# Performance work log

Hardware: AMD Instinct MI355X
Metric: run time of the kernel (lower is better)

Reference implementation:

```python
import jax, jax.numpy as jnp
import numpy as np

NX, NA, T = 128, 64, 1024
MU = 1.0          # self.mu at entry to backward_pass
EPS = 1e-8        # singular-value clamp (self.eps)


def setup_inputs() -> dict:
    key = jax.random.key(0)
    ks = jax.random.split(key, 7)
    sx = 0.3 / np.sqrt(NX)  # keep dynamics spectral norm < 1 so recursion is stable
    fx = jax.random.normal(ks[0], (T, NX, NX), dtype=jnp.float32) * sx
    fa = jax.random.normal(ks[1], (T, NX, NA), dtype=jnp.float32) * sx
    lx = jax.random.normal(ks[2], (T, NX), dtype=jnp.float32)
    la = jax.random.normal(ks[3], (T, NA), dtype=jnp.float32)
    A = jax.random.normal(ks[4], (T, NX, NX), dtype=jnp.float32) * 0.1
    lxx = 0.5 * (A + A.transpose(0, 2, 1)) + jnp.eye(NX, dtype=jnp.float32)
    B = jax.random.normal(ks[5], (T, NA, NA), dtype=jnp.float32) * 0.1
    laa = 0.5 * (B + B.transpose(0, 2, 1)) + jnp.eye(NA, dtype=jnp.float32)
    lax = jax.random.normal(ks[6], (T, NA, NX), dtype=jnp.float32) * 0.1
    return dict(fx=fx, fa=fa, lx=lx, la=la, lxx=lxx, laa=laa, lax=lax)


def reference(fx, fa, lx, la, lxx, laa, lax):
    """iLQR backward Riccati recursion (ILQR.backward_pass + ILQR.q).
    Returns gains [T, na, 1+nx]: column 0 is k (feedforward), columns 1: are K
    (feedback), ordered by ascending time t=0..T-1."""
    I = jnp.eye(NX, dtype=fx.dtype)

    def step(carry, inp):
        Vx, Vxx = carry
        fx_t, fa_t, lx_t, la_t, lxx_t, laa_t, lax_t = inp
        # Q-function expansion (ILQR.q)
        Qx = lx_t + fx_t.T @ Vx
        Qa = la_t + fa_t.T @ Vx
        Qxx = lxx_t + fx_t.T @ Vxx @ fx_t
        Vreg = Vxx + MU * I
        Qax = lax_t + fa_t.T @ Vreg @ fx_t
        Qaa = laa_t + fa_t.T @ Vreg @ fa_t
        # SVD-based regularized inverse (S[S<eps] = eps)
        U, S, Vh = jnp.linalg.svd(Qaa)
        S = jnp.maximum(S, EPS)
        Vm = Vh.T
        Qaa_inv = (Vm * (1.0 / S)) @ U.T   # V diag(1/S) U^T
        Qaa_r = (U * S) @ Vm.T             # U diag(S) V^T (reconstructed Qaa)
        k = -Qaa_inv @ Qa
        K = -Qaa_inv @ Qax
        # value-function recursion
        Vx_n = Qx + K.T @ (Qaa_r @ k) + K.T @ Qa + Qax.T @ k
        Vxx_n = Qxx + K.T @ Qaa_r @ K + K.T @ Qax + Qax.T @ K
        Vxx_n = 0.5 * (Vxx_n + Vxx_n.T)
        return (Vx_n, Vxx_n), jnp.concatenate([k[:, None], K], axis=1)

    init = (lx[-1], lxx[-1])  # terminal Vx, Vxx
    (_, _), gains = jax.lax.scan(step, init, (fx, fa, lx, la, lxx, laa, lax), reverse=True)
    return gains
```

## Files before the change

### kernel.cpp

```cpp
#include <hip/hip_runtime.h>
#include <math.h>

#define TSTEPS 1024
#define NXD 128
#define NAD 64
#define NBLK 64
#define LSTR 67
#define GAINW 129

__device__ __forceinline__ float rdl(float v, int l) {
  return __int_as_float(__builtin_amdgcn_readlane(__float_as_int(v), l));
}
__device__ __forceinline__ double rdl(double v, int l) {
  unsigned long long b = (unsigned long long)__double_as_longlong(v);
  int lo = __builtin_amdgcn_readlane((int)(b & 0xffffffffULL), l);
  int hi = __builtin_amdgcn_readlane((int)(b >> 32), l);
  unsigned long long r = (((unsigned long long)(unsigned)hi) << 32) | (unsigned)lo;
  return __longlong_as_double((long long)r);
}

__device__ __forceinline__ void gbar(unsigned* arrive, unsigned* epoch, unsigned e) {
  __syncthreads();
  if (threadIdx.x == 0) {
    unsigned prev = __hip_atomic_fetch_add(arrive, 1u, __ATOMIC_ACQ_REL, __HIP_MEMORY_SCOPE_AGENT);
    if (prev == e * NBLK - 1u) {
      __hip_atomic_store(epoch, e, __ATOMIC_RELEASE, __HIP_MEMORY_SCOPE_AGENT);
    } else {
      while (__hip_atomic_load(epoch, __ATOMIC_ACQUIRE, __HIP_MEMORY_SCOPE_AGENT) < e) {
        __builtin_amdgcn_s_sleep(1);
      }
    }
  }
  __syncthreads();
}

__device__ __forceinline__ float factor32(const float* __restrict__ QaaC, int lane,
                                          float* __restrict__ Lsh) {
  float a[64];
#pragma unroll
  for (int k = 0; k < 64; ++k) a[k] = QaaC[lane * NAD + k];
  float mmax = 0.f;
#pragma unroll
  for (int j = 0; j < 63; ++j) {
    float d = rdl(a[j], j);
    d = (d == 0.f) ? 1e-30f : d;
    float rdv = 1.0f / d;
    float m = a[j] * rdv;
    m = (lane > j) ? m : 0.f;
    mmax = fmaxf(mmax, fabsf(m));
#pragma unroll
    for (int k = j + 1; k < 64; ++k) {
      float u = rdl(a[j], k);
      a[k] = fmaf(-m, u, a[k]);
    }
    if (lane > j) a[j] = m;
  }
#pragma unroll
  for (int k = 0; k < 64; ++k) Lsh[lane * LSTR + k] = a[k];
#pragma unroll
  for (int s = 1; s < 64; s <<= 1) mmax = fmaxf(mmax, __shfl_xor(mmax, s));
  return mmax;
}

__device__ __forceinline__ void factor64(const float* __restrict__ QaaC, int lane,
                                         double* __restrict__ Lsh) {
  double a[64];
#pragma unroll
  for (int k = 0; k < 64; ++k) a[k] = (double)QaaC[lane * NAD + k];
#pragma unroll
  for (int j = 0; j < 63; ++j) {
    double d = rdl(a[j], j);
    d = (d == 0.0) ? 1e-300 : d;
    double rdv = 1.0 / d;
    double m = a[j] * rdv;
    m = (lane > j) ? m : 0.0;
#pragma unroll
    for (int k = j + 1; k < 64; ++k) {
      double u = rdl(a[j], k);
      a[k] = fma(-m, u, a[k]);
    }
    if (lane > j) a[j] = m;
  }
#pragma unroll
  for (int k = 0; k < 64; ++k) Lsh[lane * LSTR + k] = a[k];
}

template <typename T>
__device__ __forceinline__ void trisolve(const T* __restrict__ Lsh, int lane, float bval,
                                         float* __restrict__ gout, float* __restrict__ kout) {
  T x = (T)bval;
  for (int j = 0; j < 63; ++j) {
    T xj = rdl(x, j);
    T lij = Lsh[lane * LSTR + j];
    if (lane > j) x = x - lij * xj;
  }
  T d = Lsh[lane * LSTR + lane];
  if (d == (T)0) d = (T)1e-30;
  x = x / d;
  for (int j = 63; j > 0; --j) {
    T xj = rdl(x, j);
    T lji = Lsh[j * LSTR + lane];
    if (lane < j) x = x - lji * xj;
  }
  float g = -(float)x;
  *gout = g;
  *kout = g;
}

__device__ __forceinline__ void matvec128(const float* __restrict__ Vxx, float fcl, float fch,
                                          int lane, float& w0, float& w1) {
  w0 = 0.f; w1 = 0.f;
  const float* vrow = Vxx + 2 * lane;
#pragma unroll 8
  for (int c = 0; c < 64; ++c) {
    float s = rdl(fcl, c);
    float2 v = *(const float2*)(vrow + (size_t)c * NXD);
    w0 = fmaf(v.x, s, w0); w1 = fmaf(v.y, s, w1);
  }
#pragma unroll 8
  for (int c = 0; c < 64; ++c) {
    float s = rdl(fch, c);
    float2 v = *(const float2*)(vrow + (size_t)(64 + c) * NXD);
    w0 = fmaf(v.x, s, w0); w1 = fmaf(v.y, s, w1);
  }
}

__global__ void init_bar_kernel(unsigned* bar) {
  bar[threadIdx.x] = 0u;
}

__global__ __launch_bounds__(256, 1) void ilqr_main(
    const float* __restrict__ fx, const float* __restrict__ fa,
    const float* __restrict__ lx, const float* __restrict__ la,
    const float* __restrict__ lxx, const float* __restrict__ laa,
    const float* __restrict__ lax, float* __restrict__ out,
    float* __restrict__ wsf, unsigned* __restrict__ bar) {

  __shared__ float  LfS[64 * LSTR];
  __shared__ double LdS[64 * LSTR];
  __shared__ int flag64;

  const int b = blockIdx.x;
  const int tid = threadIdx.x;
  const int wave = tid >> 6;
  const int lane = tid & 63;

  float* Vxx  = wsf;
  float* Vx   = Vxx + 16384;
  float* QxxC = Vx + 128;
  float* QaxT = QxxC + 16384;
  float* QaaC = QaxT + 8192;
  float* Qx   = QaaC + 4096;
  float* Qa   = Qx + 128;
  float* KT   = Qa + 64;

  unsigned* arrive = bar;
  unsigned* epoch  = bar + 32;
  unsigned ep = 0;

  {
    const float* src = lxx + (size_t)(TSTEPS - 1) * NXD * NXD;
    int idx = b * 256 + tid;
    if (idx < NXD * NXD) Vxx[idx] = src[idx];
    if (b == 0 && tid < NXD) Vx[tid] = lx[(size_t)(TSTEPS - 1) * NXD + tid];
  }
  ++ep; gbar(arrive, epoch, ep);

  for (int t = TSTEPS - 1; t >= 0; --t) {
    const float* fxt  = fx  + (size_t)t * NXD * NXD;
    const float* fat  = fa  + (size_t)t * NXD * NAD;
    const float* lxt  = lx  + (size_t)t * NXD;
    const float* lat  = la  + (size_t)t * NAD;
    const float* lxxt = lxx + (size_t)t * NXD * NXD;
    const float* laat = laa + (size_t)t * NAD * NAD;
    const float* laxt = lax + (size_t)t * NAD * NXD;

    if (wave <= 1) {
      const int j = 2 * b + wave;
      float fcl = fxt[lane * NXD + j];
      float fch = fxt[(64 + lane) * NXD + j];
      float w0, w1;
      matvec128(Vxx, fcl, fch, lane, w0, w1);

      float q0 = lxxt[(size_t)(2 * lane) * NXD + j];
      float q1 = lxxt[(size_t)(2 * lane + 1) * NXD + j];
      float qa = laxt[lane * NXD + j];
#pragma unroll 4
      for (int r2 = 0; r2 < 32; ++r2) {
        float s0 = rdl(w0, r2), s1 = rdl(w1, r2);
        float t0 = s0 + rdl(fcl, 2 * r2);
        float t1 = s1 + rdl(fcl, 2 * r2 + 1);
        float2 f0 = *(const float2*)(fxt + (size_t)(2 * r2) * NXD + 2 * lane);
        float2 f1 = *(const float2*)(fxt + (size_t)(2 * r2 + 1) * NXD + 2 * lane);
        float g0 = fat[(2 * r2) * NAD + lane];
        float g1 = fat[(2 * r2 + 1) * NAD + lane];
        q0 = fmaf(f0.x, s0, q0); q1 = fmaf(f0.y, s0, q1);
        q0 = fmaf(f1.x, s1, q0); q1 = fmaf(f1.y, s1, q1);
        qa = fmaf(g0, t0, qa);   qa = fmaf(g1, t1, qa);
      }
#pragma unroll 4
      for (int r2 = 32; r2 < 64; ++r2) {
        float s0 = rdl(w0, r2), s1 = rdl(w1, r2);
        float t0 = s0 + rdl(fch, 2 * r2 - 64);
        float t1 = s1 + rdl(fch, 2 * r2 + 1 - 64);
        float2 f0 = *(const float2*)(fxt + (size_t)(2 * r2) * NXD + 2 * lane);
        float2 f1 = *(const float2*)(fxt + (size_t)(2 * r2 + 1) * NXD + 2 * lane);
        float g0 = fat[(2 * r2) * NAD + lane];
        float g1 = fat[(2 * r2 + 1) * NAD + lane];
        q0 = fmaf(f0.x, s0, q0); q1 = fmaf(f0.y, s0, q1);
        q0 = fmaf(f1.x, s1, q0); q1 = fmaf(f1.y, s1, q1);
        qa = fmaf(g0, t0, qa);   qa = fmaf(g1, t1, qa);
      }
      *(float2*)(QxxC + (size_t)j * NXD + 2 * lane) = make_float2(q0, q1);
      QaxT[j * NAD + lane] = qa;
    } else if (wave == 2) {
      const int j = b;
      float fcl = fat[lane * NAD + j];
      float fch = fat[(64 + lane) * NAD + j];
      float w0, w1;
      matvec128(Vxx, fcl, fch, lane, w0, w1);

      float qa = laat[lane * NAD + j];
#pragma unroll 4
      for (int r2 = 0; r2 < 32; ++r2) {
        float t0 = rdl(w0, r2) + rdl(fcl, 2 * r2);
        float t1 = rdl(w1, r2) + rdl(fcl, 2 * r2 + 1);
        float g0 = fat[(2 * r2) * NAD + lane];
        float g1 = fat[(2 * r2 + 1) * NAD + lane];
        qa = fmaf(g0, t0, qa); qa = fmaf(g1, t1, qa);
      }
#pragma unroll 4
      for (int r2 = 32; r2 < 64; ++r2) {
        float t0 = rdl(w0, r2) + rdl(fch, 2 * r2 - 64);
        float t1 = rdl(w1, r2) + rdl(fch, 2 * r2 + 1 - 64);
        float g0 = fat[(2 * r2) * NAD + lane];
        float g1 = fat[(2 * r2 + 1) * NAD + lane];
        qa = fmaf(g0, t0, qa); qa = fmaf(g1, t1, qa);
      }
      QaaC[j * NAD + lane] = qa;
    } else {
#pragma unroll
      for (int q = 0; q < 3; ++q) {
        int rr = 3 * b + q;
        float p;
        if (rr < NXD) {
          p = fxt[lane * NXD + rr] * Vx[lane] + fxt[(64 + lane) * NXD + rr] * Vx[64 + lane];
        } else {
          int aa = rr - NXD;
          p = fat[lane * NAD + aa] * Vx[lane] + fat[(64 + lane) * NAD + aa] * Vx[64 + lane];
        }
#pragma unroll
        for (int s = 1; s < 64; s <<= 1) p += __shfl_xor(p, s);
        if (lane == 0) {
          if (rr < NXD) Qx[rr] = lxt[rr] + p;
          else          Qa[rr - NXD] = lat[rr - NXD] + p;
        }
      }
    }
    ++ep; gbar(arrive, epoch, ep);

    if (wave == 0) {
      float mmax = factor32(QaaC, lane, LfS);
      if (lane == 0) flag64 = !(mmax <= 64.0f);
    }
    __syncthreads();
    if (flag64) { if (wave == 0) factor64(QaaC, lane, LdS); }
    __syncthreads();
    {
      int m = (wave == 0) ? 2 * b
            : (wave == 1) ? 2 * b + 1
            : (wave == 2 && b == 0) ? 128 : -1;
      if (m >= 0) {
        float bval = (m == 0) ? Qa[lane] : QaxT[(size_t)(m - 1) * NAD + lane];
        float* gout = out + (size_t)t * NAD * GAINW + (size_t)lane * GAINW + m;
        float* kout = KT + m * NAD + lane;
        if (!flag64) trisolve<float >(LfS, lane, bval, gout, kout);
        else         trisolve<double>(LdS, lane, bval, gout, kout);
      }
    }
    ++ep; gbar(arrive, epoch, ep);

    {
      int ti = b >> 3, tj = b & 7;
      int il = tid >> 4, jl = tid & 15;
      int i = ti * 16 + il, j = tj * 16 + jl;
      float d1 = 0.f, d2 = 0.f;
      const float* qi = QaxT + (size_t)i * NAD;
      const float* qj = QaxT + (size_t)j * NAD;
      const float* kj = KT + (size_t)(1 + j) * NAD;
      const float* ki = KT + (size_t)(1 + i) * NAD;
#pragma unroll 4
      for (int a4 = 0; a4 < 16; ++a4) {
        float4 A = *(const float4*)(qi + 4 * a4);
        float4 B = *(const float4*)(kj + 4 * a4);
        float4 C = *(const float4*)(qj + 4 * a4);
        float4 D = *(const float4*)(ki + 4 * a4);
        d1 = fmaf(A.x, B.x, d1); d1 = fmaf(A.y, B.y, d1);
        d1 = fmaf(A.z, B.z, d1); d1 = fmaf(A.w, B.w, d1);
        d2 = fmaf(C.x, D.x, d2); d2 = fmaf(C.y, D.y, d2);
        d2 = fmaf(C.z, D.z, d2); d2 = fmaf(C.w, D.w, d2);
      }
      float v = 0.5f * (QxxC[(size_t)j * NXD + i] + QxxC[(size_t)i * NXD + j])
              + 0.5f * (d1 + d2);
      Vxx[(size_t)i * NXD + j] = v;

      if (ti == tj && jl == 0) {
        float acc = 0.f;
        const float* k0 = KT;
#pragma unroll 4
        for (int a4 = 0; a4 < 16; ++a4) {
          float4 A = *(const float4*)(qi + 4 * a4);
          float4 B = *(const float4*)(k0 + 4 * a4);
          acc = fmaf(A.x, B.x, acc); acc = fmaf(A.y, B.y, acc);
          acc = fmaf(A.z, B.z, acc); acc = fmaf(A.w, B.w, acc);
        }
        Vx[i] = Qx[i] + acc;
      }
    }
    ++ep; gbar(arrive, epoch, ep);
  }
}

extern "C" void kernel_launch(void* const* d_in, const int* in_sizes, int n_in,
                              void* d_out, int out_size, void* d_ws, size_t ws_size,
                              hipStream_t stream) {
  const float* fx  = (const float*)d_in[0];
  const float* fa  = (const float*)d_in[1];
  const float* lx  = (const float*)d_in[2];
  const float* la  = (const float*)d_in[3];
  const float* lxx = (const float*)d_in[4];
  const float* laa = (const float*)d_in[5];
  const float* lax = (const float*)d_in[6];
  float* out = (float*)d_out;

  unsigned* bar = (unsigned*)d_ws;
  float* wsf = (float*)((char*)d_ws + 256);

  hipLaunchKernelGGL(init_bar_kernel, dim3(1), dim3(64), 0, stream, bar);
  hipLaunchKernelGGL(ilqr_main, dim3(NBLK), dim3(256), 0, stream,
                     fx, fa, lx, la, lxx, laa, lax, out, wsf, bar);
}
```

Measured before the change: 63.70 ms.

## Remove a grid barrier by redundantly solving needed gains per block, stage in LDS

Each block now solves its own 33 right-hand sides (the K rows it needs for its Vxx tile, plus k) with a batched triangular solve, instead of a distributed solve followed by a grid-wide barrier. This removes one of the four global barriers per time step. Vxx and Vx are staged in shared memory for the matvec, the next step's fx/fa columns are prefetched into registers, and the barrier uses relaxed atomics with explicit fences. In exchange, every block repeats the Cholesky-style factorization and nine solves, which adds compute and shared-memory pressure.

```diff
diff --git a/kernel.cpp b/kernel.cpp
--- a/kernel.cpp
+++ b/kernel.cpp
@@ -6,6 +6,8 @@
 #define NAD 64
 #define NBLK 64
 #define LSTR 67
+#define QSTR 65
+#define KSTR 68
 #define GAINW 129
 
 __device__ __forceinline__ float rdl(float v, int l) {
@@ -22,23 +24,25 @@
 __device__ __forceinline__ void gbar(unsigned* arrive, unsigned* epoch, unsigned e) {
   __syncthreads();
   if (threadIdx.x == 0) {
-    unsigned prev = __hip_atomic_fetch_add(arrive, 1u, __ATOMIC_ACQ_REL, __HIP_MEMORY_SCOPE_AGENT);
+    __builtin_amdgcn_fence(__ATOMIC_RELEASE, "agent");
+    unsigned prev = __hip_atomic_fetch_add(arrive, 1u, __ATOMIC_RELAXED, __HIP_MEMORY_SCOPE_AGENT);
     if (prev == e * NBLK - 1u) {
-      __hip_atomic_store(epoch, e, __ATOMIC_RELEASE, __HIP_MEMORY_SCOPE_AGENT);
+      __hip_atomic_store(epoch, e, __ATOMIC_RELAXED, __HIP_MEMORY_SCOPE_AGENT);
     } else {
-      while (__hip_atomic_load(epoch, __ATOMIC_ACQUIRE, __HIP_MEMORY_SCOPE_AGENT) < e) {
+      while (__hip_atomic_load(epoch, __ATOMIC_RELAXED, __HIP_MEMORY_SCOPE_AGENT) < e) {
         __builtin_amdgcn_s_sleep(1);
       }
     }
+    __builtin_amdgcn_fence(__ATOMIC_ACQUIRE, "agent");
   }
   __syncthreads();
 }
 
-__device__ __forceinline__ float factor32(const float* __restrict__ QaaC, int lane,
+__device__ __forceinline__ float factor32(const float* __restrict__ QaaS, int lane,
                                           float* __restrict__ Lsh) {
   float a[64];
 #pragma unroll
-  for (int k = 0; k < 64; ++k) a[k] = QaaC[lane * NAD + k];
+  for (int k = 0; k < 64; ++k) a[k] = QaaS[lane * QSTR + k];
   float mmax = 0.f;
 #pragma unroll
   for (int j = 0; j < 63; ++j) {
@@ -62,11 +66,11 @@
   return mmax;
 }
 
-__device__ __forceinline__ void factor64(const float* __restrict__ QaaC, int lane,
+__device__ __forceinline__ void factor64(const float* __restrict__ QaaS, int lane,
                                          double* __restrict__ Lsh) {
   double a[64];
 #pragma unroll
-  for (int k = 0; k < 64; ++k) a[k] = (double)QaaC[lane * NAD + k];
+  for (int k = 0; k < 64; ++k) a[k] = (double)QaaS[lane * QSTR + k];
 #pragma unroll
   for (int j = 0; j < 63; ++j) {
     double d = rdl(a[j], j);
@@ -86,41 +90,49 @@
 }
 
 template <typename T>
-__device__ __forceinline__ void trisolve(const T* __restrict__ Lsh, int lane, float bval,
-                                         float* __restrict__ gout, float* __restrict__ kout) {
-  T x = (T)bval;
+__device__ __forceinline__ void trisolveN(const T* __restrict__ Lsh, int lane,
+                                          const float bv[9], float g[9]) {
+  T x[9];
+#pragma unroll
+  for (int r = 0; r < 9; ++r) x[r] = (T)bv[r];
   for (int j = 0; j < 63; ++j) {
-    T xj = rdl(x, j);
     T lij = Lsh[lane * LSTR + j];
-    if (lane > j) x = x - lij * xj;
+#pragma unroll
+    for (int r = 0; r < 9; ++r) {
+      T xj = rdl(x[r], j);
+      if (lane > j) x[r] = x[r] - lij * xj;
+    }
   }
   T d = Lsh[lane * LSTR + lane];
   if (d == (T)0) d = (T)1e-30;
-  x = x / d;
+#pragma unroll
+  for (int r = 0; r < 9; ++r) x[r] = x[r] / d;
   for (int j = 63; j > 0; --j) {
-    T xj = rdl(x, j);
     T lji = Lsh[j * LSTR + lane];
-    if (lane < j) x = x - lji * xj;
-  }
-  float g = -(float)x;
-  *gout = g;
-  *kout = g;
-}
-
-__device__ __forceinline__ void matvec128(const float* __restrict__ Vxx, float fcl, float fch,
-                                          int lane, float& w0, float& w1) {
+#pragma unroll
+    for (int r = 0; r < 9; ++r) {
+      T xj = rdl(x[r], j);
+      if (lane < j) x[r] = x[r] - lji * xj;
+    }
+  }
+#pragma unroll
+  for (int r = 0; r < 9; ++r) g[r] = -(float)x[r];
+}
+
+__device__ __forceinline__ void matvec128_lds(const float* __restrict__ VxxS, float fcl, float fch,
+                                              int lane, float& w0, float& w1) {
   w0 = 0.f; w1 = 0.f;
-  const float* vrow = Vxx + 2 * lane;
+  const float* vrow = VxxS + 2 * lane;
 #pragma unroll 8
   for (int c = 0; c < 64; ++c) {
     float s = rdl(fcl, c);
-    float2 v = *(const float2*)(vrow + (size_t)c * NXD);
+    float2 v = *(const float2*)(vrow + c * NXD);
     w0 = fmaf(v.x, s, w0); w1 = fmaf(v.y, s, w1);
   }
 #pragma unroll 8
   for (int c = 0; c < 64; ++c) {
     float s = rdl(fch, c);
-    float2 v = *(const float2*)(vrow + (size_t)(64 + c) * NXD);
+    float2 v = *(const float2*)(vrow + (64 + c) * NXD);
     w0 = fmaf(v.x, s, w0); w1 = fmaf(v.y, s, w1);
   }
 }
@@ -136,14 +148,20 @@
     const float* __restrict__ lax, float* __restrict__ out,
     float* __restrict__ wsf, unsigned* __restrict__ bar) {
 
-  __shared__ float  LfS[64 * LSTR];
-  __shared__ double LdS[64 * LSTR];
+  __shared__ float  VxxS[NXD * NXD];
+  __shared__ float  VxS[NXD];
+  __shared__ float  QaaS[NAD * QSTR];
+  __shared__ float  LfS[NAD * LSTR];
+  __shared__ double LdS[NAD * LSTR];
+  __shared__ float  KS[33 * KSTR];
+  __shared__ float  QaxS[32 * KSTR];
   __shared__ int flag64;
 
   const int b = blockIdx.x;
   const int tid = threadIdx.x;
   const int wave = tid >> 6;
   const int lane = tid & 63;
+  const int ti = b >> 3, tj = b & 7;
 
   float* Vxx  = wsf;
   float* Vx   = Vxx + 16384;
@@ -152,7 +170,6 @@
   float* QaaC = QaxT + 8192;
   float* Qx   = QaaC + 4096;
   float* Qa   = Qx + 128;
-  float* KT   = Qa + 64;
 
   unsigned* arrive = bar;
   unsigned* epoch  = bar + 32;
@@ -165,6 +182,32 @@
     if (b == 0 && tid < NXD) Vx[tid] = lx[(size_t)(TSTEPS - 1) * NXD + tid];
   }
   ++ep; gbar(arrive, epoch, ep);
+
+  float pf0 = 0.f, pf1 = 0.f;
+  float pr0 = 0.f, pr1 = 0.f, pr2 = 0.f, pr3 = 0.f, pr4 = 0.f, pr5 = 0.f;
+
+  auto prefetch = [&](int tn) {
+    const float* fxn = fx + (size_t)tn * NXD * NXD;
+    const float* fan = fa + (size_t)tn * NXD * NAD;
+    if (wave <= 1) {
+      int j = 2 * b + wave;
+      pf0 = fxn[lane * NXD + j]; pf1 = fxn[(64 + lane) * NXD + j];
+    } else if (wave == 2) {
+      int j = b;
+      pf0 = fan[lane * NAD + j]; pf1 = fan[(64 + lane) * NAD + j];
+    } else {
+      int rr = 3 * b;
+      if (rr < NXD) { pr0 = fxn[lane * NXD + rr]; pr1 = fxn[(64 + lane) * NXD + rr]; }
+      else { int aa = rr - NXD; pr0 = fan[lane * NAD + aa]; pr1 = fan[(64 + lane) * NAD + aa]; }
+      rr = 3 * b + 1;
+      if (rr < NXD) { pr2 = fxn[lane * NXD + rr]; pr3 = fxn[(64 + lane) * NXD + rr]; }
+      else { int aa = rr - NXD; pr2 = fan[lane * NAD + aa]; pr3 = fan[(64 + lane) * NAD + aa]; }
+      rr = 3 * b + 2;
+      if (rr < NXD) { pr4 = fxn[lane * NXD + rr]; pr5 = fxn[(64 + lane) * NXD + rr]; }
+      else { int aa = rr - NXD; pr4 = fan[lane * NAD + aa]; pr5 = fan[(64 + lane) * NAD + aa]; }
+    }
+  };
+  prefetch(TSTEPS - 1);
 
   for (int t = TSTEPS - 1; t >= 0; --t) {
     const float* fxt  = fx  + (size_t)t * NXD * NXD;
@@ -175,12 +218,20 @@
     const float* laat = laa + (size_t)t * NAD * NAD;
     const float* laxt = lax + (size_t)t * NAD * NXD;
 
+    {
+      const float4* src = (const float4*)Vxx;
+      float4* dst = (float4*)VxxS;
+#pragma unroll
+      for (int q = 0; q < 16; ++q) dst[tid + 256 * q] = src[tid + 256 * q];
+      if (tid < NXD) VxS[tid] = Vx[tid];
+    }
+    __syncthreads();
+
     if (wave <= 1) {
       const int j = 2 * b + wave;
-      float fcl = fxt[lane * NXD + j];
-      float fch = fxt[(64 + lane) * NXD + j];
+      float fcl = pf0, fch = pf1;
       float w0, w1;
-      matvec128(Vxx, fcl, fch, lane, w0, w1);
+      matvec128_lds(VxxS, fcl, fch, lane, w0, w1);
 
       float q0 = lxxt[(size_t)(2 * lane) * NXD + j];
       float q1 = lxxt[(size_t)(2 * lane + 1) * NXD + j];
@@ -215,10 +266,9 @@
       QaxT[j * NAD + lane] = qa;
     } else if (wave == 2) {
       const int j = b;
-      float fcl = fat[lane * NAD + j];
-      float fch = fat[(64 + lane) * NAD + j];
+      float fcl = pf0, fch = pf1;
       float w0, w1;
-      matvec128(Vxx, fcl, fch, lane, w0, w1);
+      matvec128_lds(VxxS, fcl, fch, lane, w0, w1);
 
       float qa = laat[lane * NAD + j];
 #pragma unroll 4
@@ -239,16 +289,13 @@
       }
       QaaC[j * NAD + lane] = qa;
     } else {
+      float pv0 = VxS[lane], pv1 = VxS[64 + lane];
 #pragma unroll
       for (int q = 0; q < 3; ++q) {
         int rr = 3 * b + q;
-        float p;
-        if (rr < NXD) {
-          p = fxt[lane * NXD + rr] * Vx[lane] + fxt[(64 + lane) * NXD + rr] * Vx[64 + lane];
-        } else {
-          int aa = rr - NXD;
-          p = fat[lane * NAD + aa] * Vx[lane] + fat[(64 + lane) * NAD + aa] * Vx[64 + lane];
-        }
+        float f0 = (q == 0) ? pr0 : (q == 1) ? pr2 : pr4;
+        float f1 = (q == 0) ? pr1 : (q == 1) ? pr3 : pr5;
+        float p = f0 * pv0 + f1 * pv1;
 #pragma unroll
         for (int s = 1; s < 64; s <<= 1) p += __shfl_xor(p, s);
         if (lane == 0) {
@@ -259,36 +306,62 @@
     }
     ++ep; gbar(arrive, epoch, ep);
 
+    {
+#pragma unroll
+      for (int q = 0; q < 16; ++q) {
+        int idx = tid + 256 * q;
+        QaaS[(idx >> 6) * QSTR + (idx & 63)] = QaaC[idx];
+      }
+    }
+    float bv[9];
+#pragma unroll
+    for (int r = 0; r < 9; ++r) {
+      int slot = wave + 4 * r;
+      float v = 0.f;
+      if (slot < 33) {
+        int m = (slot < 16) ? (1 + 16 * tj + slot)
+              : (slot < 32) ? (1 + 16 * ti + (slot - 16)) : 0;
+        v = (slot == 32) ? Qa[lane] : QaxT[(size_t)(m - 1) * NAD + lane];
+        if (slot < 32) QaxS[slot * KSTR + lane] = v;
+      }
+      bv[r] = v;
+    }
+    __syncthreads();
     if (wave == 0) {
-      float mmax = factor32(QaaC, lane, LfS);
+      float mmax = factor32(QaaS, lane, LfS);
       if (lane == 0) flag64 = !(mmax <= 64.0f);
     }
     __syncthreads();
-    if (flag64) { if (wave == 0) factor64(QaaC, lane, LdS); }
+    if (flag64 && wave == 0) factor64(QaaS, lane, LdS);
     __syncthreads();
     {
-      int m = (wave == 0) ? 2 * b
-            : (wave == 1) ? 2 * b + 1
-            : (wave == 2 && b == 0) ? 128 : -1;
-      if (m >= 0) {
-        float bval = (m == 0) ? Qa[lane] : QaxT[(size_t)(m - 1) * NAD + lane];
-        float* gout = out + (size_t)t * NAD * GAINW + (size_t)lane * GAINW + m;
-        float* kout = KT + m * NAD + lane;
-        if (!flag64) trisolve<float >(LfS, lane, bval, gout, kout);
-        else         trisolve<double>(LdS, lane, bval, gout, kout);
-      }
-    }
-    ++ep; gbar(arrive, epoch, ep);
+      float g[9];
+      if (!flag64) trisolveN<float >(LfS, lane, bv, g);
+      else         trisolveN<double>(LdS, lane, bv, g);
+#pragma unroll
+      for (int r = 0; r < 9; ++r) {
+        int slot = wave + 4 * r;
+        if (slot < 33) {
+          KS[slot * KSTR + lane] = g[r];
+          int m = (slot < 16) ? (1 + 16 * tj + slot)
+                : (slot < 32) ? (1 + 16 * ti + (slot - 16)) : 0;
+          bool writer = (slot < 16) ? (ti == 0) : (slot == 32 && b == 0);
+          if (writer) out[(size_t)t * NAD * GAINW + (size_t)lane * GAINW + m] = g[r];
+        }
+      }
+    }
+    __syncthreads();
+
+    if (t > 0) prefetch(t - 1);
 
     {
-      int ti = b >> 3, tj = b & 7;
       int il = tid >> 4, jl = tid & 15;
       int i = ti * 16 + il, j = tj * 16 + jl;
       float d1 = 0.f, d2 = 0.f;
-      const float* qi = QaxT + (size_t)i * NAD;
-      const float* qj = QaxT + (size_t)j * NAD;
-      const float* kj = KT + (size_t)(1 + j) * NAD;
-      const float* ki = KT + (size_t)(1 + i) * NAD;
+      const float* qi = QaxS + (16 + il) * KSTR;
+      const float* qj = QaxS + jl * KSTR;
+      const float* kj = KS + jl * KSTR;
+      const float* ki = KS + (16 + il) * KSTR;
 #pragma unroll 4
       for (int a4 = 0; a4 < 16; ++a4) {
         float4 A = *(const float4*)(qi + 4 * a4);
@@ -306,7 +379,7 @@
 
       if (ti == tj && jl == 0) {
         float acc = 0.f;
-        const float* k0 = KT;
+        const float* k0 = KS + 32 * KSTR;
 #pragma unroll 4
         for (int a4 = 0; a4 < 16; ++a4) {
           float4 A = *(const float4*)(qi + 4 * a4);
```

Result: slower. 73.05 ms (+14.7%).
